# Kernel tuning notes

Measured on AMD Instinct MI355X. Metric: run time of the kernel, lower is better.

The kernel has to match this reference:

```python
import jax, jax.numpy as jnp
import numpy as np

STRIDE = 1
PADDING = 1


def setup_inputs() -> dict:
    key = jax.random.key(0)
    k1, k2 = jax.random.split(key)
    x = jax.random.normal(k1, (32, 64, 112, 112), dtype=jnp.float32)
    weights = jax.random.normal(k2, (128, 64, 3, 3), dtype=jnp.float32)
    biases = jnp.zeros((128,), dtype=jnp.float32)
    return {"x": x, "weights": weights, "biases": biases}


def reference(x, weights, biases):
    # NCHW input, OIHW weights -> NCHW output; zero padding, stride 1.
    out = jax.lax.conv_general_dilated(
        x, weights,
        window_strides=(STRIDE, STRIDE),
        padding=((PADDING, PADDING), (PADDING, PADDING)),
        dimension_numbers=("NCHW", "OIHW", "NCHW"),
    )
    return out + biases[None, :, None, None]
```

## Files before the change

### kernel.cpp

```cpp
#include <hip/hip_runtime.h>
#include <stdint.h>

typedef unsigned short u16;
typedef __attribute__((ext_vector_type(8))) short bf16x8;
typedef __attribute__((ext_vector_type(4))) float f32x4;

#define C_IN    64
#define K_OUT   128
#define HW      112
#define HW2     (HW * HW)
#define CP      72
#define NW      114
#define THREADS 256

__device__ __forceinline__ u16 f2bf(float f) {
  union { float f; uint32_t u; } x; x.f = f;
  return (u16)((x.u + 0x7FFFu + ((x.u >> 16) & 1u)) >> 16);
}

__global__ void prep_weights(const float* __restrict__ w, u16* __restrict__ wt) {
  int idx = blockIdx.x * 256 + threadIdx.x;
  if (idx >= K_OUT * C_IN * 9) return;
  int c    = idx & (C_IN - 1);
  int kout = (idx >> 6) & (K_OUT - 1);
  int rs   = idx >> 13;
  wt[idx] = f2bf(w[(kout * C_IN + c) * 9 + rs]);
}

__global__ __launch_bounds__(THREADS, 2) void conv3x3(
    const float* __restrict__ x, const u16* __restrict__ wt,
    const float* __restrict__ bias, float* __restrict__ out) {
  __shared__ u16 Xs[3][NW][CP];
  __shared__ u16 Ws[K_OUT][CP];

  const int tid = threadIdx.x;
  const int bid = blockIdx.x;
  const int n = bid / HW;
  const int h = bid % HW;

  {
    uint32_t* p = (uint32_t*)&Xs[0][0][0];
    const int tot = 3 * NW * CP / 2;
    for (int i = tid; i < tot; i += THREADS) p[i] = 0u;
  }
  __syncthreads();

  const float* xn = x + (size_t)n * C_IN * HW2;
  for (int r = 0; r < 3; ++r) {
    int row = h + r - 1;
    if (row < 0 || row >= HW) continue;
    const float* xrow = xn + (size_t)row * HW;
    for (int t = tid; t < 32 * 28; t += THREADS) {
      int w4 = t % 28;
      int cp = t / 28;
      int c  = cp * 2;
      float4 va = *(const float4*)(xrow + (size_t)c * HW2 + w4 * 4);
      float4 vb = *(const float4*)(xrow + (size_t)(c + 1) * HW2 + w4 * 4);
      int wb = 1 + w4 * 4;
      *(uint32_t*)&Xs[r][wb + 0][c] = (uint32_t)f2bf(va.x) | ((uint32_t)f2bf(vb.x) << 16);
      *(uint32_t*)&Xs[r][wb + 1][c] = (uint32_t)f2bf(va.y) | ((uint32_t)f2bf(vb.y) << 16);
      *(uint32_t*)&Xs[r][wb + 2][c] = (uint32_t)f2bf(va.z) | ((uint32_t)f2bf(vb.z) << 16);
      *(uint32_t*)&Xs[r][wb + 3][c] = (uint32_t)f2bf(va.w) | ((uint32_t)f2bf(vb.w) << 16);
    }
  }

  const int lane = tid & 63;
  const int wave = tid >> 6;
  const int quad = lane >> 4;
  const int l15  = lane & 15;
  const int kb   = wave * 32;

  f32x4 acc[2][7];
#pragma unroll
  for (int i = 0; i < 2; ++i)
#pragma unroll
    for (int j = 0; j < 7; ++j) acc[i][j] = (f32x4){0.f, 0.f, 0.f, 0.f};

  for (int rs = 0; rs < 9; ++rs) {
    const int r = rs / 3;
    const int s = rs % 3;

    __syncthreads();
    {
      const u16* wsrc = wt + rs * (K_OUT * C_IN);
#pragma unroll
      for (int t8 = 0; t8 < (K_OUT * C_IN / 8) / THREADS; ++t8) {
        int t = tid + t8 * THREADS;
        int kout = t >> 3;
        int cc = (t & 7) * 8;
        *(uint4*)&Ws[kout][cc] = *(const uint4*)(wsrc + t * 8);
      }
    }
    __syncthreads();

#pragma unroll
    for (int ch = 0; ch < 2; ++ch) {
      const int c0 = ch * 32 + quad * 8;
      bf16x8 a0 = *(const bf16x8*)&Ws[kb + l15][c0];
      bf16x8 a1 = *(const bf16x8*)&Ws[kb + 16 + l15][c0];
#pragma unroll
      for (int wt7 = 0; wt7 < 7; ++wt7) {
        bf16x8 b = *(const bf16x8*)&Xs[r][wt7 * 16 + l15 + s][c0];
        acc[0][wt7] = __builtin_amdgcn_mfma_f32_16x16x32_bf16(a0, b, acc[0][wt7], 0, 0, 0);
        acc[1][wt7] = __builtin_amdgcn_mfma_f32_16x16x32_bf16(a1, b, acc[1][wt7], 0, 0, 0);
      }
    }
  }

  float* on = out + (size_t)n * K_OUT * HW2 + (size_t)h * HW;
#pragma unroll
  for (int mt = 0; mt < 2; ++mt) {
#pragma unroll
    for (int rg = 0; rg < 4; ++rg) {
      const int kout = kb + mt * 16 + quad * 4 + rg;
      const float bv = bias[kout];
      float* orow = on + (size_t)kout * HW2;
#pragma unroll
      for (int wt7 = 0; wt7 < 7; ++wt7) {
        orow[wt7 * 16 + l15] = acc[mt][wt7][rg] + bv;
      }
    }
  }
}

extern "C" void kernel_launch(void* const* d_in, const int* in_sizes, int n_in,
                              void* d_out, int out_size, void* d_ws, size_t ws_size,
                              hipStream_t stream) {
  const float* x  = (const float*)d_in[0];
  const float* w  = (const float*)d_in[1];
  const float* bi = (const float*)d_in[2];
  float* out = (float*)d_out;
  u16* wt = (u16*)d_ws;

  prep_weights<<<(K_OUT * C_IN * 9 + 255) / 256, 256, 0, stream>>>(w, wt);
  conv3x3<<<32 * HW, THREADS, 0, stream>>>(x, wt, bi, out);
}
```

Before: 364.6 us.

## Compute two output rows per block and read weights directly from global

Each block now computes two output rows, so it loads four input rows into one shared buffer instead of three rows per output row, which cuts redundant input loads and conversion. Waves split into two row halves and two 64-channel output groups, each wave holding a 4x7 accumulator tile. The shared weight staging and its per-tap barriers are removed, and A fragments are loaded straight from global/L2. The cost is higher register pressure from 112 accumulator floats per lane, and more global weight traffic per wave that depends on caching.

```diff
diff --git a/kernel.cpp b/kernel.cpp
--- a/kernel.cpp
+++ b/kernel.cpp
@@ -10,12 +10,15 @@
 #define HW      112
 #define HW2     (HW * HW)
 #define CP      72
-#define NW      114
+#define ROWP    113
 #define THREADS 256
 
 __device__ __forceinline__ u16 f2bf(float f) {
   union { float f; uint32_t u; } x; x.f = f;
   return (u16)((x.u + 0x7FFFu + ((x.u >> 16) & 1u)) >> 16);
+}
+__device__ __forceinline__ uint32_t pack2(float lo, float hi) {
+  return (uint32_t)f2bf(lo) | ((uint32_t)f2bf(hi) << 16);
 }
 
 __global__ void prep_weights(const float* __restrict__ w, u16* __restrict__ wt) {
@@ -30,94 +33,90 @@
 __global__ __launch_bounds__(THREADS, 2) void conv3x3(
     const float* __restrict__ x, const u16* __restrict__ wt,
     const float* __restrict__ bias, float* __restrict__ out) {
-  __shared__ u16 Xs[3][NW][CP];
-  __shared__ u16 Ws[K_OUT][CP];
+  __shared__ u16 Xs[4 * ROWP + 1][CP];
 
   const int tid = threadIdx.x;
   const int bid = blockIdx.x;
-  const int n = bid / HW;
-  const int h = bid % HW;
+  const int n  = bid / (HW / 2);
+  const int h0 = (bid % (HW / 2)) * 2;
 
-  {
-    uint32_t* p = (uint32_t*)&Xs[0][0][0];
-    const int tot = 3 * NW * CP / 2;
-    for (int i = tid; i < tot; i += THREADS) p[i] = 0u;
+  if (tid < 160) {
+    int q  = tid >> 5;
+    int cp = tid & 31;
+    ((uint32_t*)&Xs[q * ROWP][0])[cp] = 0u;
+  }
+
+  const float* xn = x + (size_t)n * C_IN * HW2;
+#pragma unroll
+  for (int i = 0; i < 14; ++i) {
+    int t  = tid + i * THREADS;
+    int cp = t & 31;
+    int rest = t >> 5;
+    int w4 = rest % 28;
+    int p  = rest / 28;
+    int row = h0 - 1 + p;
+    float4 va = {0.f, 0.f, 0.f, 0.f}, vb = va;
+    if ((unsigned)row < (unsigned)HW) {
+      const float* src = xn + (size_t)(2 * cp) * HW2 + row * HW + w4 * 4;
+      va = *(const float4*)src;
+      vb = *(const float4*)(src + HW2);
+    }
+    uint32_t* dst = (uint32_t*)&Xs[p * ROWP + 1 + 4 * w4][0] + cp;
+    dst[0]   = pack2(va.x, vb.x);
+    dst[36]  = pack2(va.y, vb.y);
+    dst[72]  = pack2(va.z, vb.z);
+    dst[108] = pack2(va.w, vb.w);
   }
   __syncthreads();
 
-  const float* xn = x + (size_t)n * C_IN * HW2;
-  for (int r = 0; r < 3; ++r) {
-    int row = h + r - 1;
-    if (row < 0 || row >= HW) continue;
-    const float* xrow = xn + (size_t)row * HW;
-    for (int t = tid; t < 32 * 28; t += THREADS) {
-      int w4 = t % 28;
-      int cp = t / 28;
-      int c  = cp * 2;
-      float4 va = *(const float4*)(xrow + (size_t)c * HW2 + w4 * 4);
-      float4 vb = *(const float4*)(xrow + (size_t)(c + 1) * HW2 + w4 * 4);
-      int wb = 1 + w4 * 4;
-      *(uint32_t*)&Xs[r][wb + 0][c] = (uint32_t)f2bf(va.x) | ((uint32_t)f2bf(vb.x) << 16);
-      *(uint32_t*)&Xs[r][wb + 1][c] = (uint32_t)f2bf(va.y) | ((uint32_t)f2bf(vb.y) << 16);
-      *(uint32_t*)&Xs[r][wb + 2][c] = (uint32_t)f2bf(va.z) | ((uint32_t)f2bf(vb.z) << 16);
-      *(uint32_t*)&Xs[r][wb + 3][c] = (uint32_t)f2bf(va.w) | ((uint32_t)f2bf(vb.w) << 16);
-    }
-  }
+  const int lane  = tid & 63;
+  const int wave  = tid >> 6;
+  const int quad  = lane >> 4;
+  const int l15   = lane & 15;
+  const int h_sub = wave >> 1;
+  const int kb    = (wave & 1) * 64;
 
-  const int lane = tid & 63;
-  const int wave = tid >> 6;
-  const int quad = lane >> 4;
-  const int l15  = lane & 15;
-  const int kb   = wave * 32;
-
-  f32x4 acc[2][7];
+  f32x4 acc[4][7];
 #pragma unroll
-  for (int i = 0; i < 2; ++i)
+  for (int i = 0; i < 4; ++i)
 #pragma unroll
     for (int j = 0; j < 7; ++j) acc[i][j] = (f32x4){0.f, 0.f, 0.f, 0.f};
 
+#pragma unroll
   for (int rs = 0; rs < 9; ++rs) {
-    const int r = rs / 3;
-    const int s = rs % 3;
-
-    __syncthreads();
-    {
-      const u16* wsrc = wt + rs * (K_OUT * C_IN);
-#pragma unroll
-      for (int t8 = 0; t8 < (K_OUT * C_IN / 8) / THREADS; ++t8) {
-        int t = tid + t8 * THREADS;
-        int kout = t >> 3;
-        int cc = (t & 7) * 8;
-        *(uint4*)&Ws[kout][cc] = *(const uint4*)(wsrc + t * 8);
-      }
-    }
-    __syncthreads();
-
+    const int r = rs / 3, s = rs % 3;
+    const u16* wbase = wt + (size_t)(rs * K_OUT + kb + l15) * C_IN;
+    const int xrow0 = (h_sub + r) * ROWP + s;
 #pragma unroll
     for (int ch = 0; ch < 2; ++ch) {
       const int c0 = ch * 32 + quad * 8;
-      bf16x8 a0 = *(const bf16x8*)&Ws[kb + l15][c0];
-      bf16x8 a1 = *(const bf16x8*)&Ws[kb + 16 + l15][c0];
+      bf16x8 a0 = *(const bf16x8*)(wbase + c0);
+      bf16x8 a1 = *(const bf16x8*)(wbase + 16 * C_IN + c0);
+      bf16x8 a2 = *(const bf16x8*)(wbase + 32 * C_IN + c0);
+      bf16x8 a3 = *(const bf16x8*)(wbase + 48 * C_IN + c0);
 #pragma unroll
-      for (int wt7 = 0; wt7 < 7; ++wt7) {
-        bf16x8 b = *(const bf16x8*)&Xs[r][wt7 * 16 + l15 + s][c0];
-        acc[0][wt7] = __builtin_amdgcn_mfma_f32_16x16x32_bf16(a0, b, acc[0][wt7], 0, 0, 0);
-        acc[1][wt7] = __builtin_amdgcn_mfma_f32_16x16x32_bf16(a1, b, acc[1][wt7], 0, 0, 0);
+      for (int w7 = 0; w7 < 7; ++w7) {
+        bf16x8 b = *(const bf16x8*)&Xs[xrow0 + w7 * 16 + l15][c0];
+        acc[0][w7] = __builtin_amdgcn_mfma_f32_16x16x32_bf16(a0, b, acc[0][w7], 0, 0, 0);
+        acc[1][w7] = __builtin_amdgcn_mfma_f32_16x16x32_bf16(a1, b, acc[1][w7], 0, 0, 0);
+        acc[2][w7] = __builtin_amdgcn_mfma_f32_16x16x32_bf16(a2, b, acc[2][w7], 0, 0, 0);
+        acc[3][w7] = __builtin_amdgcn_mfma_f32_16x16x32_bf16(a3, b, acc[3][w7], 0, 0, 0);
       }
     }
   }
 
-  float* on = out + (size_t)n * K_OUT * HW2 + (size_t)h * HW;
+  const int h = h0 + h_sub;
+  float* obase = out + ((size_t)n * K_OUT + kb) * HW2 + h * HW + l15;
 #pragma unroll
-  for (int mt = 0; mt < 2; ++mt) {
+  for (int mt = 0; mt < 4; ++mt) {
 #pragma unroll
     for (int rg = 0; rg < 4; ++rg) {
-      const int kout = kb + mt * 16 + quad * 4 + rg;
-      const float bv = bias[kout];
-      float* orow = on + (size_t)kout * HW2;
+      const int kl = mt * 16 + quad * 4 + rg;
+      const float bv = bias[kb + kl];
+      float* orow = obase + (size_t)kl * HW2;
 #pragma unroll
-      for (int wt7 = 0; wt7 < 7; ++wt7) {
-        orow[wt7 * 16 + l15] = acc[mt][wt7][rg] + bv;
+      for (int w7 = 0; w7 < 7; ++w7) {
+        orow[w7 * 16] = acc[mt][w7][rg] + bv;
       }
     }
   }
@@ -133,5 +132,5 @@
   u16* wt = (u16*)d_ws;
 
   prep_weights<<<(K_OUT * C_IN * 9 + 255) / 256, 256, 0, stream>>>(w, wt);
-  conv3x3<<<32 * HW, THREADS, 0, stream>>>(x, wt, bi, out);
+  conv3x3<<<32 * (HW / 2), THREADS, 0, stream>>>(x, wt, bi, out);
 }
```

Measured after the change: 368.5 us. No clear change (+1.1%).
